# Kernel optimization log

Hardware: AMD Instinct MI355X
Metric: run time of the kernel (lower is better)

## Reference

```python
import jax, jax.numpy as jnp
import numpy as np
from jax import lax

NEG = -1e30  # finite stand-in for -inf so logaddexp grads stay finite


def setup_inputs() -> dict:
    key = jax.random.key(0)
    k1, k2, k3, k4, k5 = jax.random.split(key, 5)
    B, T, L, S = 16, 2048, 256, 8
    return {
        "emissions": jax.random.normal(k1, (B, T, S), dtype=jnp.float32),
        "transition": jax.random.normal(k2, (S, S), dtype=jnp.float32),
        "bos": jax.random.normal(k3, (S,), dtype=jnp.float32),
        "eos": jax.random.normal(k4, (S,), dtype=jnp.float32),
        "lengths": jnp.full((B,), T, dtype=jnp.int32),
        "targets": jax.random.randint(k5, (B, L), 0, 4, dtype=jnp.int32),
        "target_lengths": jnp.full((B,), L, dtype=jnp.int32),
    }


def _den_logz(em, lengths, transition, bos, eos):
    # Exact log-semiring forward over the fully-connected 8-state denominator CRF graph
    # (the limit of k2.intersect_dense_pruned(...).get_tot_scores(log_semiring=True)).
    B, T, S = em.shape
    alpha0 = bos[None, :] + em[:, 0, :]  # (B,S)

    def step(alpha, em_t):
        a = jax.nn.logsumexp(alpha[:, :, None] + transition[None, :, :], axis=1) + em_t
        return a, a

    _, alphas = lax.scan(step, alpha0, jnp.swapaxes(em, 0, 1)[1:])  # (T-1,B,S)
    alphas = jnp.concatenate([alpha0[None], alphas], axis=0)  # (T,B,S)
    fin = alphas[lengths - 1, jnp.arange(B)]  # (B,S) alpha at last valid frame
    return jax.nn.logsumexp(fin + eos[None, :], axis=-1)


def _num_logz(em, lengths, targets, target_lengths, transition, bos, eos):
    # Forward over the target-constrained enter/extend lattice: symbol u must be
    # entered (state targets[u]) exactly once, optionally extended (state targets[u]+4),
    # then the path moves monotonically to symbol u+1.
    B, T, S = em.shape
    L = targets.shape[1]
    b_idx = jnp.arange(B)
    es = targets          # enter-state ids, (B,L)
    xs = targets + 4      # extend-state ids, (B,L)

    t_xx = transition[xs, xs]  # extend_u -> extend_u
    t_ex = transition[es, xs]  # enter_u  -> extend_u
    prev_e = jnp.concatenate([es[:, :1], es[:, :-1]], axis=1)
    prev_x = jnp.concatenate([xs[:, :1], xs[:, :-1]], axis=1)
    t_ee = transition[prev_e, es]  # enter_{u-1}  -> enter_u
    t_xe = transition[prev_x, es]  # extend_{u-1} -> enter_u

    a_e0 = jnp.full((B, L), NEG, dtype=em.dtype)
    a_e0 = a_e0.at[:, 0].set(bos[es[:, 0]] + em[b_idx, 0, es[:, 0]])
    a_x0 = jnp.full((B, L), NEG, dtype=em.dtype)

    def shift(a):  # a[:, u-1], NEG at u=0
        return jnp.concatenate([jnp.full((B, 1), NEG, dtype=a.dtype), a[:, :-1]], axis=1)

    def step(carry, em_t):
        a_e, a_x = carry
        em_e = jnp.take_along_axis(em_t, es, axis=1)  # (B,L)
        em_x = jnp.take_along_axis(em_t, xs, axis=1)
        new_e = em_e + jnp.logaddexp(shift(a_e) + t_ee, shift(a_x) + t_xe)
        new_x = em_x + jnp.logaddexp(a_e + t_ex, a_x + t_xx)
        return (new_e, new_x), (new_e, new_x)

    _, (ae, ax) = lax.scan(step, (a_e0, a_x0), jnp.swapaxes(em, 0, 1)[1:])
    ae = jnp.concatenate([a_e0[None], ae], axis=0)  # (T,B,L)
    ax = jnp.concatenate([a_x0[None], ax], axis=0)
    fin_e = ae[lengths - 1, b_idx]  # (B,L)
    fin_x = ax[lengths - 1, b_idx]
    u = target_lengths - 1
    fe = fin_e[b_idx, u] + eos[es[b_idx, u]]
    fx = fin_x[b_idx, u] + eos[xs[b_idx, u]]
    return jnp.logaddexp(fe, fx)  # (B,)


def reference(emissions, transition, bos, eos, lengths, targets, target_lengths):
    em = emissions.astype(jnp.float32)
    logz_den = _den_logz(em, lengths, transition, bos, eos)
    logz_num = _num_logz(em, lengths, targets, target_lengths, transition, bos, eos)
    # all samples valid by construction (lengths > 0, 0 < target_len <= length)
    return jnp.mean(logz_den - logz_num)
```

## Files before the change

kernel.cpp:

```cpp
#include <hip/hip_runtime.h>
#include <math.h>


#define LOG2E 1.4426950408889634f
#define LN2   0.69314718055994531f
#define CTL_WSHL1  0x130
#define CTL_WSHR1  0x138
#define CTL_ROR(r) (0x120 + (r))

#define AST(p, v) __hip_atomic_store((p), (v), __ATOMIC_RELAXED, __HIP_MEMORY_SCOPE_AGENT)
#define ALD(p)    __hip_atomic_load((p), __ATOMIC_RELAXED, __HIP_MEMORY_SCOPE_AGENT)

template <int CTRL>
__device__ __forceinline__ float fdpp(float x) {
    return __int_as_float(__builtin_amdgcn_update_dpp(
        0, __float_as_int(x), CTRL, 0xF, 0xF, true));
}
template <int CTRL>
__device__ __forceinline__ int idpp(int x) {
    return __builtin_amdgcn_update_dpp(0, x, CTRL, 0xF, 0xF, true);
}

__device__ __forceinline__ void pin() {
#if __has_builtin(__builtin_amdgcn_sched_barrier)
    __builtin_amdgcn_sched_barrier(0);
#else
    asm volatile("" ::: "memory");
#endif
}

__device__ __forceinline__ float fexp2(float x) {
#if __has_builtin(__builtin_amdgcn_exp2f)
    return __builtin_amdgcn_exp2f(x);
#else
    return exp2f(x);
#endif
}
__device__ __forceinline__ float flog2(float x) {
#if __has_builtin(__builtin_amdgcn_logf)
    return __builtin_amdgcn_logf(x);
#else
    return __log2f(x);
#endif
}
__device__ __forceinline__ float lse2(float a, float b) {
    float m = fmaxf(a, b);
    float d = fminf(a, b) - m;
    return m + flog2(1.0f + fexp2(d));
}

#define NFW_STEP {                                                          \
    float2 q0 = st0[tb + k + 1], q1 = st1[tb + k + 1];                      \
    float2 rv = make_float2(0.0f, 0.0f);                                    \
    if (CONS) rv = rEX[k * 64 + 63];                                        \
    float nbE = fdpp<CTL_WSHR1>(E[1]);                                      \
    float nbX = fdpp<CTL_WSHR1>(X[1]);                                      \
    if (CONS && l0) { nbE = rv.x; nbX = rv.y; }                             \
    float nE0 = p0.x * fmaf(nbE,  teeF, nbX  * txeF);                       \
    float nE1 = p1.x * fmaf(E[0], tee1, X[0] * txe1);                       \
    float nX0 = p0.y * fmaf(E[0], tex0, X[0] * txx0);                       \
    float nX1 = p1.y * fmaf(E[1], tex1, X[1] * txx1);                       \
    E[0] = nE0; E[1] = nE1; X[0] = nX0; X[1] = nX1;                         \
    if (!CONS) rEX[(k + 1) * 64 + lane] = make_float2(E[1], X[1]);          \
    if ((k & 7) == 7) {                                                     \
        int rs = 0;                                                         \
        if (CONS) rs = rS[(k >> 3) * 64 + 63];                              \
        float m = fmaxf(fmaxf(E[0], E[1]), fmaxf(X[0], X[1]));              \
        const bool live = (m > 0.0f);                                       \
        const int ex = live ? ((int)(__float_as_uint(m) >> 23) - 126) : 0;  \
        s += ex;                                                            \
        int bs = idpp<CTL_WSHR1>(s);                                        \
        if (CONS && l0) bs = rs;                                            \
        if (!live) s = bs;                                                  \
        int d = (g == 0) ? 0 : (bs - s);                                    \
        const int extra = (d > 30) ? d : 0;                                 \
        s += extra; d -= extra;                                             \
        const float fsc = ldexpf(1.0f, -(ex + extra));                      \
        E[0] *= fsc; E[1] *= fsc; X[0] *= fsc; X[1] *= fsc;                 \
        const float fs0 = (g == 0) ? 0.0f : ldexpf(1.0f, d);                \
        teeF = tee0 * fs0; txeF = txe0 * fs0;                               \
        if (!CONS) { rS[(k >> 3) * 64 + lane] = s;                          \
                     rEX[(k + 1) * 64 + lane] = make_float2(E[1], X[1]); }  \
    }                                                                       \
    p0 = q0; p1 = q1; }

template <bool CONS>
__device__ __forceinline__ void nfwd_chunk(
    const float2* st0, const float2* st1,
    float (&E)[2], float (&X)[2], int& s, float& teeF, float& txeF,
    float tee0, float txe0, float tee1, float txe1,
    float tex0, float txx0, float tex1, float txx1,
    int tb, int n, int g, int lane, float2* rEX, int* rS)
{
    const bool l0 = (lane == 0);
    if (!CONS) rEX[lane] = make_float2(E[1], X[1]);
    float2 p0 = st0[tb], p1 = st1[tb];
    if (n == 16) {
#pragma unroll
        for (int k = 0; k < 16; ++k) NFW_STEP
    } else {
        for (int k = 0; k < n; ++k) NFW_STEP
    }
}

#define NBW_STEP {                                                          \
    float2 q0 = st0[tb - k - 1], q1 = st1[tb - k - 1];                      \
    float rm = 0.0f;                                                        \
    if (CONS) rm = rM[k * 64];                                              \
    float mm0 = p0.x * bE[0];                                               \
    float mm1 = p1.x * bE[1];                                               \
    float m10 = p0.y * bX[0];                                               \
    float m11 = p1.y * bX[1];                                               \
    float mup = fdpp<CTL_WSHL1>(mm0);                                       \
    if (CONS && l63) mup = rm;                                              \
    if (!CONS) rM[k * 64 + lane] = mm0;                                     \
    float nE0 = fmaf(tex0, m10, teeN0 * mm1);                               \
    float nX0 = fmaf(txx0, m10, txeN0 * mm1);                               \
    float nE1 = fmaf(tex1, m11, teeN1F * mup);                              \
    float nX1 = fmaf(txx1, m11, txeN1F * mup);                              \
    bE[0] = nE0; bE[1] = nE1; bX[0] = nX0; bX[1] = nX1;                     \
    if ((k & 7) == 7) {                                                     \
        int rs = 0;                                                         \
        if (CONS) rs = rS[(k >> 3) * 64];                                   \
        float m = fmaxf(fmaxf(bE[0], bE[1]), fmaxf(bX[0], bX[1]));          \
        const bool live = (m > 0.0f);                                       \
        const int ex = live ? ((int)(__float_as_uint(m) >> 23) - 126) : 0;  \
        s += ex;                                                            \
        int bs = idpp<CTL_WSHL1>(s);                                        \
        if (CONS && l63) bs = rs;                                           \
        if (!live) s = bs;                                                  \
        int d = (g == 127) ? 0 : (bs - s);                                  \
        const int extra = (d > 30) ? d : 0;                                 \
        s += extra; d -= extra;                                             \
        const float fsc = ldexpf(1.0f, -(ex + extra));                      \
        bE[0] *= fsc; bE[1] *= fsc; bX[0] *= fsc; bX[1] *= fsc;             \
        const float fs = (g == 127) ? 0.0f : ldexpf(1.0f, d);               \
        teeN1F = teeN1 * fs; txeN1F = txeN1 * fs;                           \
        if (!CONS) rS[(k >> 3) * 64 + lane] = s;                            \
    }                                                                       \
    p0 = q0; p1 = q1; }

template <bool CONS>
__device__ __forceinline__ void nbwd_chunk(
    const float2* st0, const float2* st1,
    float (&bE)[2], float (&bX)[2], int& s, float& teeN1F, float& txeN1F,
    float teeN0, float txeN0, float teeN1, float txeN1,
    float tex0, float txx0, float tex1, float txx1,
    int tb, int n, int g, int lane, float* rM, int* rS)
{
    const bool l63 = (lane == 63);
    float2 p0 = st0[tb], p1 = st1[tb];
    if (n == 16) {
#pragma unroll
        for (int k = 0; k < 16; ++k) NBW_STEP
    } else {
        for (int k = 0; k < n; ++k) NBW_STEP
    }
}

__device__ __forceinline__ float denf_step(float al, float emt, const float* Tr) {
    float v1 = fdpp<CTL_ROR(1)>(al);
    float v2 = fdpp<CTL_ROR(2)>(al);
    float v3 = fdpp<CTL_ROR(3)>(al);
    float v4 = fdpp<CTL_ROR(4)>(al);
    float v5 = fdpp<CTL_ROR(5)>(al);
    float v6 = fdpp<CTL_ROR(6)>(al);
    float v7 = fdpp<CTL_ROR(7)>(al);
    float q0 = fmaf(v1, Tr[1], al * Tr[0]);
    float q1 = fmaf(v3, Tr[3], v2 * Tr[2]);
    float q2 = fmaf(v5, Tr[5], v4 * Tr[4]);
    float q3 = fmaf(v7, Tr[7], v6 * Tr[6]);
    return ((q0 + q1) + (q2 + q3)) * emt;
}
__device__ __forceinline__ float denb_step(float al, float emt, const float* TrB) {
    float g  = al * emt;
    float v1 = fdpp<CTL_ROR(7)>(g);
    float v2 = fdpp<CTL_ROR(6)>(g);
    float v3 = fdpp<CTL_ROR(5)>(g);
    float v4 = fdpp<CTL_ROR(4)>(g);
    float v5 = fdpp<CTL_ROR(3)>(g);
    float v6 = fdpp<CTL_ROR(2)>(g);
    float v7 = fdpp<CTL_ROR(1)>(g);
    float q0 = fmaf(v1, TrB[1], g * TrB[0]);
    float q1 = fmaf(v3, TrB[3], v2 * TrB[2]);
    float q2 = fmaf(v5, TrB[5], v4 * TrB[4]);
    float q3 = fmaf(v7, TrB[7], v6 * TrB[6]);
    return (q0 + q1) + (q2 + q3);
}
__device__ __forceinline__ int den_renorm(float& al) {
    float mm = fmaxf(al, fdpp<CTL_ROR(4)>(al));
    mm = fmaxf(mm, fdpp<CTL_ROR(2)>(mm));
    mm = fmaxf(mm, fdpp<CTL_ROR(1)>(mm));
    const int ex = (int)(__float_as_uint(mm) >> 23) - 126;
    al = ldexpf(al, -ex);
    return ex;
}

extern "C" __global__ void __launch_bounds__(128)
crf_fused(const float* __restrict__ em, const float* __restrict__ trans,
          const float* __restrict__ bos, const float* __restrict__ eos,
          const int* __restrict__ lengths, const int* __restrict__ targets,
          const int* __restrict__ tlens,
          float* __restrict__ ws, float* __restrict__ out,
          int B, int T, int S, int L)
{
    extern __shared__ float sm[];
    const int bid  = blockIdx.x;
    const int tid  = threadIdx.x;
    const int lane = tid & 63;
    const int wv   = tid >> 6;
    const int half = S >> 1;
    const int role = bid / B;
    const int b    = bid % B;
    const float* gem = em + (size_t)b * T * S;
    const int len = lengths[b];
    const int tm  = (len - 1) >> 1;
    const int P2  = T + 2;
    const int RINGF = 8 * P2;

    float* NF  = ws + 16 + (size_t)b * 640;
    float* NB  = ws + 16 + (size_t)B * 640 + (size_t)b * 640;
    float* DEN = ws + 16 + (size_t)(2 * B) * 640;
    int* ticket = (int*)ws;

    if (role < 2) {
        float2* s2 = (float2*)sm;
        for (int t = tid; t < T; t += 128) {
            const float4* gr = (const float4*)(gem + t * S);
            float4 a = gr[0], c4 = gr[1];
            s2[0 * P2 + t] = make_float2(fexp2(a.x * LOG2E), fexp2(c4.x * LOG2E));
            s2[1 * P2 + t] = make_float2(fexp2(a.y * LOG2E), fexp2(c4.y * LOG2E));
            s2[2 * P2 + t] = make_float2(fexp2(a.z * LOG2E), fexp2(c4.z * LOG2E));
            s2[3 * P2 + t] = make_float2(fexp2(a.w * LOG2E), fexp2(c4.w * LOG2E));
        }
    } else {
        for (int t = tid; t < T; t += 128) {
            const float4* gr = (const float4*)(gem + t * S);
            float4 a = gr[0], c4 = gr[1];
            float4 w0, w1;
            w0.x = fexp2(a.x * LOG2E); w0.y = fexp2(c4.x * LOG2E);
            w0.z = fexp2(a.y * LOG2E); w0.w = fexp2(c4.y * LOG2E);
            w1.x = fexp2(a.z * LOG2E); w1.y = fexp2(c4.z * LOG2E);
            w1.z = fexp2(a.w * LOG2E); w1.w = fexp2(c4.w * LOG2E);
            ((float4*)sm)[t * 2]     = w0;
            ((float4*)sm)[t * 2 + 1] = w1;
        }
    }
    __syncthreads();

    if (role == 0) {
        const float2* s2v = (const float2*)sm;
        const int g   = (wv << 6) + lane;
        const int u0g = g * 2;
        const int base = b * L;
        const int e0 = targets[base + ((u0g     < L) ? u0g     : (L - 1))];
        const int e1 = targets[base + ((u0g + 1 < L) ? u0g + 1 : (L - 1))];
        const int ep = (u0g > 0) ? targets[base + u0g - 1] : e0;
        const float tee0 = fexp2(trans[ep * S + e0] * LOG2E);
        const float txe0 = fexp2(trans[(ep + half) * S + e0] * LOG2E);
        const float tee1 = fexp2(trans[e0 * S + e1] * LOG2E);
        const float txe1 = fexp2(trans[(e0 + half) * S + e1] * LOG2E);
        const float tex0 = fexp2(trans[e0 * S + e0 + half] * LOG2E);
        const float txx0 = fexp2(trans[(e0 + half) * S + e0 + half] * LOG2E);
        const float tex1 = fexp2(trans[e1 * S + e1 + half] * LOG2E);
        const float txx1 = fexp2(trans[(e1 + half) * S + e1 + half] * LOG2E);
        const float2* st0 = s2v + e0 * P2;
        const float2* st1 = s2v + e1 * P2;
        float E[2] = {0.f, 0.f}, X[2] = {0.f, 0.f};
        int s = 0;
        if (g == 0) E[0] = fexp2(bos[e0] * LOG2E) * st0[0].x;
        float teeF = (g == 0) ? 0.0f : tee0;
        float txeF = (g == 0) ? 0.0f : txe0;

        float2* ringEX = (float2*)(sm + RINGF);
        int*    ringS  = (int*)(sm + RINGF + 4352);
        const int NCH = (tm + 15) >> 4;
        for (int ph = 0; ph <= NCH; ++ph) {
            const int ci = (wv == 0) ? ph : ph - 1;
            if (ci >= 0 && ci < NCH) {
                const int tb = 1 + (ci << 4);
                int n = tm - tb + 1; if (n > 16) n = 16;
                float2* rEX = ringEX + (ci & 1) * (17 * 64);
                int*    rS  = ringS  + (ci & 1) * 128;
                if (wv == 0)
                    nfwd_chunk<false>(st0, st1, E, X, s, teeF, txeF,
                                      tee0, txe0, tee1, txe1,
                                      tex0, txx0, tex1, txx1,
                                      tb, n, g, lane, rEX, rS);
                else
                    nfwd_chunk<true>(st0, st1, E, X, s, teeF, txeF,
                                     tee0, txe0, tee1, txe1,
                                     tex0, txx0, tex1, txx1,
                                     tb, n, g, lane, rEX, rS);
            }
            __syncthreads();
        }
        AST(&NF[g * 4 + 0], E[0]);
        AST(&NF[g * 4 + 1], E[1]);
        AST(&NF[g * 4 + 2], X[0]);
        AST(&NF[g * 4 + 3], X[1]);
        AST(&NF[512 + g], __int_as_float(s));
    } else if (role == 1) {
        const float2* s2v = (const float2*)sm;
        const int g   = (wv << 6) + lane;
        const int u0g = g * 2;
        const int base = b * L;
        const int e0 = targets[base + ((u0g     < L) ? u0g     : (L - 1))];
        const int e1 = targets[base + ((u0g + 1 < L) ? u0g + 1 : (L - 1))];
        const int e2 = targets[base + ((u0g + 2 < L) ? u0g + 2 : (L - 1))];
        const float tex0 = fexp2(trans[e0 * S + e0 + half] * LOG2E);
        const float txx0 = fexp2(trans[(e0 + half) * S + e0 + half] * LOG2E);
        const float tex1 = fexp2(trans[e1 * S + e1 + half] * LOG2E);
        const float txx1 = fexp2(trans[(e1 + half) * S + e1 + half] * LOG2E);
        const float teeN0 = fexp2(trans[e0 * S + e1] * LOG2E);
        const float txeN0 = fexp2(trans[(e0 + half) * S + e1] * LOG2E);
        float teeN1 = fexp2(trans[e1 * S + e2] * LOG2E);
        float txeN1 = fexp2(trans[(e1 + half) * S + e2] * LOG2E);
        if (g == 127) { teeN1 = 0.0f; txeN1 = 0.0f; }
        const float2* st0 = s2v + e0 * P2;
        const float2* st1 = s2v + e1 * P2;
        float bE[2] = {0.f, 0.f}, bX[2] = {0.f, 0.f};
        const int uf = tlens[b] - 1;
        if (g == (uf >> 1)) {
            const int kf = uf & 1;
            const int ef = kf ? e1 : e0;
            bE[kf] = fexp2(eos[ef] * LOG2E);
            bX[kf] = fexp2(eos[ef + half] * LOG2E);
        }
        int s = 0;
        float teeN1F = teeN1, txeN1F = txeN1;

        float* ringM = sm + RINGF;
        int*   ringS = (int*)(sm + RINGF + 4352);
        const int th = len - 1, tlo = tm + 1;
        const int nbs = th - tlo + 1;
        const int NCH = (nbs > 0) ? ((nbs + 15) >> 4) : 0;
        for (int ph = 0; ph <= NCH; ++ph) {
            const int ci = (wv == 1) ? ph : ph - 1;
            if (ci >= 0 && ci < NCH) {
                const int tb = th - (ci << 4);
                int n = tb - tlo + 1; if (n > 16) n = 16;
                float* rM = ringM + (ci & 1) * 1024;
                int*   rS = ringS + (ci & 1) * 128;
                if (wv == 1)
                    nbwd_chunk<false>(st0, st1, bE, bX, s, teeN1F, txeN1F,
                                      teeN0, txeN0, teeN1, txeN1,
                                      tex0, txx0, tex1, txx1,
                                      tb, n, g, lane, rM, rS);
                else
                    nbwd_chunk<true>(st0, st1, bE, bX, s, teeN1F, txeN1F,
                                     teeN0, txeN0, teeN1, txeN1,
                                     tex0, txx0, tex1, txx1,
                                     tb, n, g, lane, rM, rS);
            }
            __syncthreads();
        }
        AST(&NB[g * 4 + 0], bE[0]);
        AST(&NB[g * 4 + 1], bE[1]);
        AST(&NB[g * 4 + 2], bX[0]);
        AST(&NB[g * 4 + 3], bX[1]);
        AST(&NB[512 + g], __int_as_float(s));
    } else {
        float* denF  = sm + T * 8 + 16;
        float* denB  = denF + 8;
        int*   denFs = (int*)(denB + 8);
        int*   denBs = denFs + 8;
        const int j  = lane & 7;
        const int jj = ((j & 3) << 1) + (j >> 2);
        if (wv == 0) {
            float Tr[8];
#pragma unroll
            for (int r = 0; r < 8; ++r)
                Tr[r] = fexp2(trans[((j - r) & 7) * S + j] * LOG2E);
            float al = fexp2(bos[j] * LOG2E) * sm[jj];
            int sc = 0;
            int t = 1;
            if (t + 3 <= tm) {
                float c0 = sm[t * 8 + jj];
                float c1 = sm[(t + 1) * 8 + jj];
                float c2 = sm[(t + 2) * 8 + jj];
                float c3 = sm[(t + 3) * 8 + jj];
                pin();
                while (t + 7 <= tm) {
                    float d0 = sm[(t + 4) * 8 + jj];
                    float d1 = sm[(t + 5) * 8 + jj];
                    float d2 = sm[(t + 6) * 8 + jj];
                    float d3 = sm[(t + 7) * 8 + jj];
                    pin();
                    al = denf_step(al, c0, Tr);
                    al = denf_step(al, c1, Tr);
                    al = denf_step(al, c2, Tr);
                    al = denf_step(al, c3, Tr);
                    sc += den_renorm(al);
                    c0 = d0; c1 = d1; c2 = d2; c3 = d3;
                    t += 4;
                }
                al = denf_step(al, c0, Tr);
                al = denf_step(al, c1, Tr);
                al = denf_step(al, c2, Tr);
                al = denf_step(al, c3, Tr);
                sc += den_renorm(al);
                t += 4;
            }
            while (t <= tm) { al = denf_step(al, sm[t * 8 + jj], Tr); ++t; }
            if (lane < 8) { denF[j] = al; denFs[j] = sc; }
        } else {
            float TrB[8];
#pragma unroll
            for (int r = 0; r < 8; ++r)
                TrB[r] = fexp2(trans[j * S + ((j + r) & 7)] * LOG2E);
            float al = fexp2(eos[j] * LOG2E);
            int sc = 0;
            int t = len - 1;
            const int tlo = tm + 1;
            if (t - 3 >= tlo) {
                float c0 = sm[t * 8 + jj];
                float c1 = sm[(t - 1) * 8 + jj];
                float c2 = sm[(t - 2) * 8 + jj];
                float c3 = sm[(t - 3) * 8 + jj];
                pin();
                while (t - 7 >= tlo) {
                    float d0 = sm[(t - 4) * 8 + jj];
                    float d1 = sm[(t - 5) * 8 + jj];
                    float d2 = sm[(t - 6) * 8 + jj];
                    float d3 = sm[(t - 7) * 8 + jj];
                    pin();
                    al = denb_step(al, c0, TrB);
                    al = denb_step(al, c1, TrB);
                    al = denb_step(al, c2, TrB);
                    al = denb_step(al, c3, TrB);
                    sc += den_renorm(al);
                    c0 = d0; c1 = d1; c2 = d2; c3 = d3;
                    t -= 4;
                }
                al = denb_step(al, c0, TrB);
                al = denb_step(al, c1, TrB);
                al = denb_step(al, c2, TrB);
                al = denb_step(al, c3, TrB);
                sc += den_renorm(al);
                t -= 4;
            }
            while (t >= tlo) { al = denb_step(al, sm[t * 8 + jj], TrB); --t; }
            if (lane < 8) { denB[j] = al; denBs[j] = sc; }
        }
        __syncthreads();
        if (wv == 0 && lane < 8) {
            const float a  = fmaxf(denF[j], 1e-37f);
            const float bb = fmaxf(denB[j], 1e-37f);
            float part = flog2(a) + flog2(bb) + (float)(denFs[j] + denBs[j]);
            part = lse2(part, __shfl_xor(part, 1, 64));
            part = lse2(part, __shfl_xor(part, 2, 64));
            part = lse2(part, __shfl_xor(part, 4, 64));
            if (j == 0) AST(&DEN[b], part);
        }
    }

    __syncthreads();
    int* wflag = (int*)sm;
    if (tid == 0) {
        __threadfence();
        const int tk = atomicAdd(ticket, 1);
        wflag[0] = (tk == 3 * B - 1) ? 1 : 0;
    }
    __syncthreads();
    if (wflag[0] && tid < 64) {
        __threadfence();
        float acc = 0.0f;
        for (int bb2 = 0; bb2 < B; ++bb2) {
            const float* nf = ws + 16 + (size_t)bb2 * 640;
            const float* nb = ws + 16 + (size_t)B * 640 + (size_t)bb2 * 640;
            float va = 0.0f, vb = 0.0f;
#pragma unroll
            for (int k = 0; k < 4; ++k)
                va = fmaf(ALD(&nf[lane * 4 + k]), ALD(&nb[lane * 4 + k]), va);
#pragma unroll
            for (int k = 0; k < 4; ++k)
                vb = fmaf(ALD(&nf[256 + lane * 4 + k]),
                          ALD(&nb[256 + lane * 4 + k]), vb);
            const int sa = __float_as_int(ALD(&nf[512 + lane]))
                         + __float_as_int(ALD(&nb[512 + lane]));
            const int sb = __float_as_int(ALD(&nf[576 + lane]))
                         + __float_as_int(ALD(&nb[576 + lane]));
            float pa = (va > 0.0f) ? (flog2(va) + (float)sa) : -3.0e38f;
            float pb = (vb > 0.0f) ? (flog2(vb) + (float)sb) : -3.0e38f;
            float part = lse2(pa, pb);
#pragma unroll
            for (int o = 1; o < 64; o <<= 1)
                part = lse2(part, __shfl_xor(part, o, 64));
            if (lane == 0) acc += ALD(&DEN[bb2]) - part;
        }
        if (lane == 0) out[0] = acc * (LN2 / (float)B);
    }
}

extern "C" void kernel_launch(void* const* d_in, const int* in_sizes, int n_in,
                              void* d_out, int out_size, void* d_ws, size_t ws_size,
                              hipStream_t stream)
{
    const float* em      = (const float*)d_in[0];
    const float* trans   = (const float*)d_in[1];
    const float* bos     = (const float*)d_in[2];
    const float* eos     = (const float*)d_in[3];
    const int*   lengths = (const int*)d_in[4];
    const int*   targets = (const int*)d_in[5];
    const int*   tlens   = (const int*)d_in[6];
    float* out = (float*)d_out;
    float* ws  = (float*)d_ws;

    const int B  = in_sizes[4];
    const int SS = in_sizes[1];
    int S = 1; while (S * S < SS) ++S;
    const int T = in_sizes[0] / (B * S);
    const int L = in_sizes[5] / B;

    const size_t shmem = (size_t)(8 * (T + 2) + 4352 + 256) * sizeof(float);

    static bool attr_done = false;
    if (!attr_done) {
        (void)hipFuncSetAttribute((const void*)crf_fused,
                                  hipFuncAttributeMaxDynamicSharedMemorySize,
                                  (int)(96 * 1024));
        attr_done = true;
    }

    (void)hipMemsetAsync(ws, 0, 64, stream);
    hipLaunchKernelGGL(crf_fused, dim3(3 * B), dim3(128), shmem, stream,
                       em, trans, bos, eos, lengths, targets, tlens,
                       ws, out, B, T, S, L);
}
```

Measured before the change: 150.8 us.

## Split denominator forward/backward chains into quarters via transfer-matrix blocks

The denominator CRF chain per batch element was processed as a forward half and a backward half. It is now split into four segments. Two new block roles propagate all 8 unit-vector basis states through the middle segments to build 8x8 transfer matrices, with per-column scale exponents. The final reducer combines the quarter-length alpha/beta vectors with these matrices, shortening the serial dependency chain. The cost is launching 5B blocks instead of 3B, extra workspace traffic, and a more complex final combination with per-column scale alignment.

```diff
diff --git a/kernel.cpp b/kernel.cpp
--- a/kernel.cpp
+++ b/kernel.cpp
@@ -220,8 +220,14 @@
 
     float* NF  = ws + 16 + (size_t)b * 640;
     float* NB  = ws + 16 + (size_t)B * 640 + (size_t)b * 640;
-    float* DEN = ws + 16 + (size_t)(2 * B) * 640;
+    const size_t DENR = 16 + (size_t)(2 * B) * 640;
+    const size_t MATF = DENR + (size_t)B * 32;
+    const size_t MATB = MATF + (size_t)B * 128;
     int* ticket = (int*)ws;
+
+    const int tq  = tm >> 1;
+    const int dlo = tm + 1, dhi = len - 1;
+    const int tq2 = (dhi >= dlo) ? (dlo + ((dhi - dlo) >> 1)) : (dlo - 1);
 
     if (role < 2) {
         float2* s2 = (float2*)sm;
@@ -360,11 +366,8 @@
         AST(&NB[g * 4 + 2], bX[0]);
         AST(&NB[g * 4 + 3], bX[1]);
         AST(&NB[512 + g], __int_as_float(s));
-    } else {
-        float* denF  = sm + T * 8 + 16;
-        float* denB  = denF + 8;
-        int*   denFs = (int*)(denB + 8);
-        int*   denBs = denFs + 8;
+    } else if (role == 2) {
+        float* DR = ws + DENR + (size_t)b * 32;
         const int j  = lane & 7;
         const int jj = ((j & 3) << 1) + (j >> 2);
         if (wv == 0) {
@@ -375,13 +378,13 @@
             float al = fexp2(bos[j] * LOG2E) * sm[jj];
             int sc = 0;
             int t = 1;
-            if (t + 3 <= tm) {
+            if (t + 3 <= tq) {
                 float c0 = sm[t * 8 + jj];
                 float c1 = sm[(t + 1) * 8 + jj];
                 float c2 = sm[(t + 2) * 8 + jj];
                 float c3 = sm[(t + 3) * 8 + jj];
                 pin();
-                while (t + 7 <= tm) {
+                while (t + 7 <= tq) {
                     float d0 = sm[(t + 4) * 8 + jj];
                     float d1 = sm[(t + 5) * 8 + jj];
                     float d2 = sm[(t + 6) * 8 + jj];
@@ -402,8 +405,11 @@
                 sc += den_renorm(al);
                 t += 4;
             }
-            while (t <= tm) { al = denf_step(al, sm[t * 8 + jj], Tr); ++t; }
-            if (lane < 8) { denF[j] = al; denFs[j] = sc; }
+            while (t <= tq) { al = denf_step(al, sm[t * 8 + jj], Tr); ++t; }
+            if (lane < 8) {
+                AST(&DR[j], al);
+                if (j == 0) AST(&DR[8], __int_as_float(sc));
+            }
         } else {
             float TrB[8];
 #pragma unroll
@@ -411,15 +417,15 @@
                 TrB[r] = fexp2(trans[j * S + ((j + r) & 7)] * LOG2E);
             float al = fexp2(eos[j] * LOG2E);
             int sc = 0;
-            int t = len - 1;
-            const int tlo = tm + 1;
-            if (t - 3 >= tlo) {
+            int t = dhi;
+            const int tloR = tq2 + 1;
+            if (t - 3 >= tloR) {
                 float c0 = sm[t * 8 + jj];
                 float c1 = sm[(t - 1) * 8 + jj];
                 float c2 = sm[(t - 2) * 8 + jj];
                 float c3 = sm[(t - 3) * 8 + jj];
                 pin();
-                while (t - 7 >= tlo) {
+                while (t - 7 >= tloR) {
                     float d0 = sm[(t - 4) * 8 + jj];
                     float d1 = sm[(t - 5) * 8 + jj];
                     float d2 = sm[(t - 6) * 8 + jj];
@@ -440,18 +446,99 @@
                 sc += den_renorm(al);
                 t -= 4;
             }
-            while (t >= tlo) { al = denb_step(al, sm[t * 8 + jj], TrB); --t; }
-            if (lane < 8) { denB[j] = al; denBs[j] = sc; }
-        }
-        __syncthreads();
-        if (wv == 0 && lane < 8) {
-            const float a  = fmaxf(denF[j], 1e-37f);
-            const float bb = fmaxf(denB[j], 1e-37f);
-            float part = flog2(a) + flog2(bb) + (float)(denFs[j] + denBs[j]);
-            part = lse2(part, __shfl_xor(part, 1, 64));
-            part = lse2(part, __shfl_xor(part, 2, 64));
-            part = lse2(part, __shfl_xor(part, 4, 64));
-            if (j == 0) AST(&DEN[b], part);
+            while (t >= tloR) { al = denb_step(al, sm[t * 8 + jj], TrB); --t; }
+            if (lane < 8) {
+                AST(&DR[16 + j], al);
+                if (j == 0) AST(&DR[24], __int_as_float(sc));
+            }
+        }
+    } else if (role == 3) {
+        float* MF = ws + MATF + (size_t)b * 128;
+        const int j  = lane & 7;
+        const int jj = ((j & 3) << 1) + (j >> 2);
+        const int cc = (wv << 2) + (lane >> 4);
+        float Tr[8];
+#pragma unroll
+        for (int r = 0; r < 8; ++r)
+            Tr[r] = fexp2(trans[((j - r) & 7) * S + j] * LOG2E);
+        float al = (j == cc) ? 1.0f : 0.0f;
+        int sc = 0;
+        int t = tq + 1;
+        if (t + 3 <= tm) {
+            float c0 = sm[t * 8 + jj];
+            float c1 = sm[(t + 1) * 8 + jj];
+            float c2 = sm[(t + 2) * 8 + jj];
+            float c3 = sm[(t + 3) * 8 + jj];
+            pin();
+            while (t + 7 <= tm) {
+                float d0 = sm[(t + 4) * 8 + jj];
+                float d1 = sm[(t + 5) * 8 + jj];
+                float d2 = sm[(t + 6) * 8 + jj];
+                float d3 = sm[(t + 7) * 8 + jj];
+                pin();
+                al = denf_step(al, c0, Tr);
+                al = denf_step(al, c1, Tr);
+                al = denf_step(al, c2, Tr);
+                al = denf_step(al, c3, Tr);
+                sc += den_renorm(al);
+                c0 = d0; c1 = d1; c2 = d2; c3 = d3;
+                t += 4;
+            }
+            al = denf_step(al, c0, Tr);
+            al = denf_step(al, c1, Tr);
+            al = denf_step(al, c2, Tr);
+            al = denf_step(al, c3, Tr);
+            sc += den_renorm(al);
+            t += 4;
+        }
+        while (t <= tm) { al = denf_step(al, sm[t * 8 + jj], Tr); ++t; }
+        if ((lane & 15) < 8) {
+            AST(&MF[cc * 8 + j], al);
+            if (j == 0) AST(&MF[64 + cc], __int_as_float(sc));
+        }
+    } else {
+        float* MB = ws + MATB + (size_t)b * 128;
+        const int j  = lane & 7;
+        const int jj = ((j & 3) << 1) + (j >> 2);
+        const int cc = (wv << 2) + (lane >> 4);
+        float TrB[8];
+#pragma unroll
+        for (int r = 0; r < 8; ++r)
+            TrB[r] = fexp2(trans[j * S + ((j + r) & 7)] * LOG2E);
+        float al = (j == cc) ? 1.0f : 0.0f;
+        int sc = 0;
+        int t = tq2;
+        if (t - 3 >= dlo) {
+            float c0 = sm[t * 8 + jj];
+            float c1 = sm[(t - 1) * 8 + jj];
+            float c2 = sm[(t - 2) * 8 + jj];
+            float c3 = sm[(t - 3) * 8 + jj];
+            pin();
+            while (t - 7 >= dlo) {
+                float d0 = sm[(t - 4) * 8 + jj];
+                float d1 = sm[(t - 5) * 8 + jj];
+                float d2 = sm[(t - 6) * 8 + jj];
+                float d3 = sm[(t - 7) * 8 + jj];
+                pin();
+                al = denb_step(al, c0, TrB);
+                al = denb_step(al, c1, TrB);
+                al = denb_step(al, c2, TrB);
+                al = denb_step(al, c3, TrB);
+                sc += den_renorm(al);
+                c0 = d0; c1 = d1; c2 = d2; c3 = d3;
+                t -= 4;
+            }
+            al = denb_step(al, c0, TrB);
+            al = denb_step(al, c1, TrB);
+            al = denb_step(al, c2, TrB);
+            al = denb_step(al, c3, TrB);
+            sc += den_renorm(al);
+            t -= 4;
+        }
+        while (t >= dlo) { al = denb_step(al, sm[t * 8 + jj], TrB); --t; }
+        if ((lane & 15) < 8) {
+            AST(&MB[cc * 8 + j], al);
+            if (j == 0) AST(&MB[64 + cc], __int_as_float(sc));
         }
     }
 
@@ -460,12 +547,13 @@
     if (tid == 0) {
         __threadfence();
         const int tk = atomicAdd(ticket, 1);
-        wflag[0] = (tk == 3 * B - 1) ? 1 : 0;
+        wflag[0] = (tk == 5 * B - 1) ? 1 : 0;
     }
     __syncthreads();
     if (wflag[0] && tid < 64) {
         __threadfence();
         float acc = 0.0f;
+        const int c8 = lane >> 3, j8 = lane & 7;
         for (int bb2 = 0; bb2 < B; ++bb2) {
             const float* nf = ws + 16 + (size_t)bb2 * 640;
             const float* nb = ws + 16 + (size_t)B * 640 + (size_t)bb2 * 640;
@@ -487,7 +575,40 @@
 #pragma unroll
             for (int o = 1; o < 64; o <<= 1)
                 part = lse2(part, __shfl_xor(part, o, 64));
-            if (lane == 0) acc += ALD(&DEN[bb2]) - part;
+
+            const float* dr = ws + DENR + (size_t)bb2 * 32;
+            const float* mf = ws + MATF + (size_t)bb2 * 128;
+            const float* mb = ws + MATB + (size_t)bb2 * 128;
+            int s1 = __float_as_int(ALD(&mf[64 + c8]));
+            int m1 = s1;
+#pragma unroll
+            for (int o = 8; o < 64; o <<= 1) {
+                int oth = __shfl_xor(m1, o, 64);
+                m1 = (oth > m1) ? oth : m1;
+            }
+            int s2 = __float_as_int(ALD(&mb[64 + c8]));
+            int m2 = s2;
+#pragma unroll
+            for (int o = 8; o < 64; o <<= 1) {
+                int oth = __shfl_xor(m2, o, 64);
+                m2 = (oth > m2) ? oth : m2;
+            }
+            float t1 = ALD(&dr[c8]) * ALD(&mf[c8 * 8 + j8])
+                     * ldexpf(1.0f, s1 - m1);
+#pragma unroll
+            for (int o = 8; o < 64; o <<= 1) t1 += __shfl_xor(t1, o, 64);
+            float t2 = ALD(&dr[16 + c8]) * ALD(&mb[c8 * 8 + j8])
+                     * ldexpf(1.0f, s2 - m2);
+#pragma unroll
+            for (int o = 8; o < 64; o <<= 1) t2 += __shfl_xor(t2, o, 64);
+            float pd = t1 * t2;
+#pragma unroll
+            for (int o = 1; o < 8; o <<= 1) pd += __shfl_xor(pd, o, 64);
+            const int scF = __float_as_int(ALD(&dr[8]));
+            const int scB = __float_as_int(ALD(&dr[24]));
+            float logden = flog2(fmaxf(pd, 1e-37f))
+                         + (float)(scF + scB + m1 + m2);
+            if (lane == 0) acc += logden - part;
         }
         if (lane == 0) out[0] = acc * (LN2 / (float)B);
     }
@@ -524,7 +645,7 @@
     }
 
     (void)hipMemsetAsync(ws, 0, 64, stream);
-    hipLaunchKernelGGL(crf_fused, dim3(3 * B), dim3(128), shmem, stream,
+    hipLaunchKernelGGL(crf_fused, dim3(5 * B), dim3(128), shmem, stream,
                        em, trans, bos, eos, lengths, targets, tlens,
                        ws, out, B, T, S, L);
 }
```

New measurement: 153.1 us. Within noise of the previous version (+1.5%).
